# Kernel tuning notes

Hardware: AMD Instinct MI355X
Metric: run time of the kernel (lower is better)

Reference implementation:

```python
import jax, jax.numpy as jnp
import numpy as np

BN_EPS = 1e-3          # nn.BatchNorm1d(..., eps=0.001)
NUM_PILLARS = 600000   # M = total occupied pillars across the batch
N_POINTS = 3_000_000
C_IN, C_OUT = 10, 64


def setup_inputs() -> dict:
    key = jax.random.key(0)
    k1, k2, k3 = jax.random.split(key, 3)
    pts_feature = jax.random.normal(k1, (N_POINTS, C_IN), dtype=jnp.float32)
    point_pillar_indices = jax.random.randint(k2, (N_POINTS,), 0, NUM_PILLARS, dtype=jnp.int32)
    # Linear(C_IN, C_OUT, bias=False), kaiming_normal init
    W = jax.random.normal(k3, (C_IN, C_OUT), dtype=jnp.float32) * np.sqrt(2.0 / C_IN)
    # BatchNorm1d in eval mode (running stats)
    gamma = jnp.ones((C_OUT,), jnp.float32)
    beta = jnp.zeros((C_OUT,), jnp.float32)
    run_mean = jnp.zeros((C_OUT,), jnp.float32)
    run_var = jnp.ones((C_OUT,), jnp.float32)
    return {"pts_feature": pts_feature, "point_pillar_indices": point_pillar_indices,
            "W": W, "gamma": gamma, "beta": beta, "run_mean": run_mean, "run_var": run_var}


def reference(pts_feature, point_pillar_indices, W, gamma, beta, run_mean, run_var):
    # shared MLP: Linear(no bias) -> BatchNorm1d(eval) -> ReLU, fused per-point
    h = pts_feature @ W                                        # (N, C_OUT)
    h = gamma * (h - run_mean) * jax.lax.rsqrt(run_var + BN_EPS) + beta
    h = jax.nn.relu(h)
    # scatter_max over irregular pillar ids -> (M, C_OUT)
    pooled = jax.ops.segment_max(h, point_pillar_indices, num_segments=NUM_PILLARS)
    # torch scatter_max leaves empty pillars at 0; jax gives -inf -> replace
    return jnp.where(jnp.isfinite(pooled), pooled, 0.0)
```

## Files before the change

kernel.cpp:

```cpp
#include <hip/hip_runtime.h>
#include <hip/hip_bf16.h>

#define C_IN 10
#define C_OUT 64
#define BN_EPS 1e-3f

#define BPF   256
#define CB    256
#define NBMAX 4704
#define TS    2048
#define MAXT  2048

typedef __attribute__((ext_vector_type(8))) short bf16x8;
typedef __attribute__((ext_vector_type(4))) float f32x4;


__global__ __launch_bounds__(1024) void k1_hist(const int* __restrict__ idx, int n, int chunk,
                                                unsigned* __restrict__ ghist, int NB, int shift) {
    __shared__ unsigned h[NBMAX];
    const int b = blockIdx.x, t = threadIdx.x;
    for (int i = t; i < NB; i += 1024) h[i] = 0u;
    __syncthreads();
    const int lo = b * chunk;
    const int hi = min(n, lo + chunk);
    for (int i = lo + t; i < hi; i += 1024)
        atomicAdd(&h[((unsigned)idx[i]) >> shift], 1u);
    __syncthreads();
    for (int k = t; k < NB; k += 1024) ghist[(size_t)k * CB + b] = h[k];
}

__global__ __launch_bounds__(256) void k2a_reduce(const unsigned* __restrict__ g, int G,
                                                  unsigned* __restrict__ tsum) {
    __shared__ unsigned s[256];
    const int t = threadIdx.x;
    const int base = blockIdx.x * TS + t * 8;
    unsigned acc = 0;
#pragma unroll
    for (int j = 0; j < 8; ++j) { int gi = base + j; if (gi < G) acc += g[gi]; }
    s[t] = acc; __syncthreads();
    for (int off = 128; off > 0; off >>= 1) { if (t < off) s[t] += s[t + off]; __syncthreads(); }
    if (t == 0) tsum[blockIdx.x] = s[0];
}

__global__ __launch_bounds__(256) void k2b_scan(unsigned* __restrict__ tsum, int nt) {
    __shared__ unsigned partial[256], basev[256];
    const int t = threadIdx.x;
    const int per = (nt + 255) / 256;
    const int lo = t * per, hi = min(nt, lo + per);
    unsigned s = 0;
    for (int i = lo; i < hi; ++i) s += tsum[i];
    partial[t] = s; __syncthreads();
    if (t == 0) { unsigned a = 0; for (int k = 0; k < 256; ++k) { basev[k] = a; a += partial[k]; } }
    __syncthreads();
    unsigned a = basev[t];
    for (int i = lo; i < hi; ++i) { unsigned v = tsum[i]; tsum[i] = a; a += v; }
}

__global__ __launch_bounds__(256) void k2c_apply(unsigned* __restrict__ g, int G,
                                                 const unsigned* __restrict__ tsum,
                                                 unsigned* __restrict__ bstart, int NB, int n) {
    __shared__ unsigned s[256];
    const int t = threadIdx.x;
    const int base = blockIdx.x * TS + t * 8;
    unsigned v[8]; unsigned acc = 0;
#pragma unroll
    for (int j = 0; j < 8; ++j) { int gi = base + j; v[j] = (gi < G) ? g[gi] : 0u; acc += v[j]; }
    s[t] = acc; __syncthreads();
    for (int off = 1; off < 256; off <<= 1) {
        unsigned x = (t >= off) ? s[t - off] : 0u; __syncthreads();
        s[t] += x; __syncthreads();
    }
    unsigned excl = ((t == 0) ? 0u : s[t - 1]) + tsum[blockIdx.x];
#pragma unroll
    for (int j = 0; j < 8; ++j) {
        int gi = base + j;
        if (gi < G) {
            g[gi] = excl;
            if ((gi & (CB - 1)) == 0) bstart[gi / CB] = excl;
            excl += v[j];
        }
    }
    if (blockIdx.x == 0 && t == 0) bstart[NB] = (unsigned)n;
}

__global__ __launch_bounds__(1024) void k3_scatter(const int* __restrict__ idx, int n, int chunk,
                                                   const unsigned* __restrict__ scanned,
                                                   unsigned* __restrict__ rec, int NB,
                                                   int shift, unsigned lpmask) {
    __shared__ unsigned cnt[NBMAX];
    __shared__ unsigned basel[NBMAX];
    const int b = blockIdx.x, t = threadIdx.x;
    for (int k = t; k < NB; k += 1024) { basel[k] = scanned[(size_t)k * CB + b]; cnt[k] = 0u; }
    __syncthreads();
    const int lo = b * chunk, hi = min(n, lo + chunk);
    for (int i = lo + t; i < hi; i += 1024) {
        unsigned pid = (unsigned)idx[i];
        unsigned k = pid >> shift;
        unsigned r = atomicAdd(&cnt[k], 1u);
        rec[basel[k] + r] = ((pid & lpmask) << 22) | (unsigned)i;
    }
}

static __device__ __forceinline__ unsigned pk2(float2 v) {
    __hip_bfloat162 h = __float22bfloat162_rn(v);
    return *reinterpret_cast<unsigned*>(&h);
}

__global__ __launch_bounds__(1024) void pool_sfm_kernel(
    const float* __restrict__ pts,
    const unsigned* __restrict__ rec,
    const unsigned* __restrict__ bstart,
    const float* __restrict__ W,
    const float* __restrict__ gamma, const float* __restrict__ beta,
    const float* __restrict__ mean, const float* __restrict__ var,
    float* __restrict__ out, int M)
{
    __shared__ unsigned smax[BPF * C_OUT];
    __shared__ unsigned short ord[MAXT + 16];
    __shared__ unsigned lps32[(MAXT + 16) / 4];
    __shared__ unsigned cnt[BPF];
    __shared__ unsigned cur[BPF];
    __shared__ unsigned wsum[4];
    unsigned char* lpsb = (unsigned char*)lps32;

    const int b = blockIdx.x, t = threadIdx.x;
    const int lane = t & 63, w = t >> 6;
    const int g = lane >> 4, c0 = lane & 15;

    {
        uint4* s4 = (uint4*)smax;
        const uint4 z = make_uint4(0u, 0u, 0u, 0u);
        for (int i = t; i < BPF * C_OUT / 4; i += 1024) s4[i] = z;
    }
    if (t < BPF) cnt[t] = 0u;

    bf16x8 bfrag[4];
#pragma unroll
    for (int tc = 0; tc < 4; ++tc) {
        const int ch = 16 * tc + c0;
        const float sc = gamma[ch] * rsqrtf(var[ch] + BN_EPS);
        const float sh = fmaf(-mean[ch], sc, beta[ch]);
        union { bf16x8 v; unsigned short u[8]; } B;
#pragma unroll
        for (int j = 0; j < 8; ++j) {
            const int k = g * 8 + j;
            float val = 0.f;
            if (k < 10) val = W[k * C_OUT + ch] * sc;
            else if (k == 10) val = sh;
            __hip_bfloat16 hb = __float2bfloat16(val);
            B.u[j] = *reinterpret_cast<unsigned short*>(&hb);
        }
        bfrag[tc] = B.v;
    }

    const unsigned base = bstart[b];
    const int T  = (int)(bstart[b + 1] - base);
    const int Tc = T < MAXT ? T : MAXT;
    __syncthreads();

    int l0i = -1, l1i = -1;
    if (t < Tc)        { l0i = (int)(rec[base + t] >> 22);        atomicAdd(&cnt[l0i], 1u); }
    if (t + 1024 < Tc) { l1i = (int)(rec[base + t + 1024] >> 22); atomicAdd(&cnt[l1i], 1u); }
    __syncthreads();
    unsigned myv = 0, mys = 0;
    if (t < BPF) {
        myv = cnt[t];
        mys = myv;
#pragma unroll
        for (int off = 1; off < 64; off <<= 1) {
            unsigned y = (unsigned)__shfl_up((int)mys, off);
            if (lane >= off) mys += y;
        }
        if (lane == 63) wsum[t >> 6] = mys;
    }
    __syncthreads();
    if (t < BPF) {
        unsigned add = 0;
        const int mw = t >> 6;
        if (mw > 0) add += wsum[0];
        if (mw > 1) add += wsum[1];
        if (mw > 2) add += wsum[2];
        cur[t] = mys - myv + add;
    }
    __syncthreads();
    if (l0i >= 0) { unsigned p = atomicAdd(&cur[l0i], 1u); ord[p] = (unsigned short)t;          lpsb[p] = (unsigned char)l0i; }
    if (l1i >= 0) { unsigned p = atomicAdd(&cur[l1i], 1u); ord[p] = (unsigned short)(t + 1024); lpsb[p] = (unsigned char)l1i; }
    __syncthreads();
    const int nt16 = (Tc + 15) >> 4;
    {
        const int padn = nt16 * 16 - Tc;
        if (Tc > 0 && t < padn) { ord[Tc + t] = ord[Tc - 1]; lpsb[Tc + t] = lpsb[Tc - 1]; }
    }
    __syncthreads();

    int tile = w;
    unsigned rcB = 0u;
    float2 x0p, x1p, x2p, x3p, x4p;
    x0p = x1p = x2p = x3p = x4p = make_float2(0.f, 0.f);
    if (tile < nt16) {
        const int o = (int)ord[(tile << 4) + c0];
        const unsigned rcA = rec[base + o];
        const float2* fp = (const float2*)(pts + (size_t)(rcA & 0x3FFFFFu) * C_IN);
        if (g == 0)      { x0p = fp[0]; x1p = fp[1]; x2p = fp[2]; x3p = fp[3]; }
        else if (g == 1) { x4p = fp[4]; }
    }
    if (tile + 16 < nt16) {
        const int o = (int)ord[((tile + 16) << 4) + c0];
        rcB = rec[base + o];
    }

    for (; tile < nt16; tile += 16) {
        const int tb = tile << 4;
        const float2 x0 = x0p, x1 = x1p, x2 = x2p, x3 = x3p, x4 = x4p;

        unsigned rcC = 0u;
        if (tile + 32 < nt16) {
            const int o = (int)ord[((tile + 32) << 4) + c0];
            rcC = rec[base + o];
        }
        if (tile + 16 < nt16) {
            const float2* fp = (const float2*)(pts + (size_t)(rcB & 0x3FFFFFu) * C_IN);
            if (g == 0)      { x0p = fp[0]; x1p = fp[1]; x2p = fp[2]; x3p = fp[3]; }
            else if (g == 1) { x4p = fp[4]; }
        }
        rcB = rcC;

        uint4 Aq;
        if (g == 0)      Aq = make_uint4(pk2(x0), pk2(x1), pk2(x2), pk2(x3));
        else if (g == 1) Aq = make_uint4(pk2(x4), 0x00003F80u, 0u, 0u);
        else             Aq = make_uint4(0u, 0u, 0u, 0u);
        union { uint4 q; bf16x8 v; } A; A.q = Aq;

        const unsigned L = *(const unsigned*)(lpsb + tb + (g << 2));

        const f32x4 z4 = {0.f, 0.f, 0.f, 0.f};
        f32x4 a0 = __builtin_amdgcn_mfma_f32_16x16x32_bf16(A.v, bfrag[0], z4, 0, 0, 0);
        f32x4 a1 = __builtin_amdgcn_mfma_f32_16x16x32_bf16(A.v, bfrag[1], z4, 0, 0, 0);
        f32x4 a2 = __builtin_amdgcn_mfma_f32_16x16x32_bf16(A.v, bfrag[2], z4, 0, 0, 0);
        f32x4 a3 = __builtin_amdgcn_mfma_f32_16x16x32_bf16(A.v, bfrag[3], z4, 0, 0, 0);

        const int lp0 = (int)(L & 255u), lp1 = (int)((L >> 8) & 255u),
                  lp2 = (int)((L >> 16) & 255u), lp3 = (int)((L >> 24) & 255u);
        float m0 = a0[0], m1 = a1[0], m2 = a2[0], m3 = a3[0];
        int cp = lp0;
#define FLUSHM() { \
        unsigned* rowp = &smax[((unsigned)cp) << 6]; \
        const unsigned rb = (unsigned)(c0 + cp); \
        atomicMax(&rowp[(rb      ) & 63u], __float_as_uint(fmaxf(m0, 0.f))); \
        atomicMax(&rowp[(rb + 16u) & 63u], __float_as_uint(fmaxf(m1, 0.f))); \
        atomicMax(&rowp[(rb + 32u) & 63u], __float_as_uint(fmaxf(m2, 0.f))); \
        atomicMax(&rowp[(rb + 48u) & 63u], __float_as_uint(fmaxf(m3, 0.f))); }
        if (lp1 == cp) { m0 = fmaxf(m0, a0[1]); m1 = fmaxf(m1, a1[1]); m2 = fmaxf(m2, a2[1]); m3 = fmaxf(m3, a3[1]); }
        else { FLUSHM(); m0 = a0[1]; m1 = a1[1]; m2 = a2[1]; m3 = a3[1]; cp = lp1; }
        if (lp2 == cp) { m0 = fmaxf(m0, a0[2]); m1 = fmaxf(m1, a1[2]); m2 = fmaxf(m2, a2[2]); m3 = fmaxf(m3, a3[2]); }
        else { FLUSHM(); m0 = a0[2]; m1 = a1[2]; m2 = a2[2]; m3 = a3[2]; cp = lp2; }
        if (lp3 == cp) { m0 = fmaxf(m0, a0[3]); m1 = fmaxf(m1, a1[3]); m2 = fmaxf(m2, a2[3]); m3 = fmaxf(m3, a3[3]); }
        else { FLUSHM(); m0 = a0[3]; m1 = a1[3]; m2 = a2[3]; m3 = a3[3]; cp = lp3; }
        FLUSHM();
#undef FLUSHM
    }
    __syncthreads();

    for (int row = w; row < BPF; row += 16) {
        const int gp = b * BPF + row;
        if (gp < M)
            out[(size_t)gp * C_OUT + lane] = __uint_as_float(smax[row * 64 + ((lane + row) & 63)]);
    }

    if (T > MAXT) {
        __syncthreads();
        for (int r = MAXT + w; r < T; r += 16) {
            const unsigned rc = rec[base + r];
            const float* fp = pts + (size_t)(rc & 0x3FFFFFu) * C_IN;
            float h = 0.f;
#pragma unroll
            for (int j = 0; j < C_IN; ++j) h = fmaf(fp[j], W[j * C_OUT + lane], h);
            const float sc = gamma[lane] * rsqrtf(var[lane] + BN_EPS);
            h = fmaxf(fmaf(h, sc, fmaf(-mean[lane], sc, beta[lane])), 0.f);
            const int gp = b * BPF + (int)(rc >> 22);
            atomicMax((unsigned*)&out[(size_t)gp * C_OUT + lane], __float_as_uint(h));
        }
    }
}

__global__ __launch_bounds__(256) void zero_out_kernel(float4* __restrict__ out4, int n4) {
    int i = blockIdx.x * blockDim.x + threadIdx.x;
    int stride = gridDim.x * blockDim.x;
    float4 z = make_float4(0.f, 0.f, 0.f, 0.f);
    for (int j = i; j < n4; j += stride) out4[j] = z;
}

__global__ __launch_bounds__(256) void pillar_scatter_kernel(
    const float* __restrict__ pts, const int* __restrict__ idx,
    const float* __restrict__ W, const float* __restrict__ gamma,
    const float* __restrict__ beta, const float* __restrict__ mean,
    const float* __restrict__ var, unsigned int* __restrict__ out, int npoints)
{
    const int lane = threadIdx.x & 63;
    float wv[C_IN];
#pragma unroll
    for (int j = 0; j < C_IN; ++j) wv[j] = W[j * C_OUT + lane];
    const float scale = gamma[lane] * rsqrtf(var[lane] + BN_EPS);
    const float shift = fmaf(-mean[lane], scale, beta[lane]);
    const int wave_id = (blockIdx.x * blockDim.x + threadIdx.x) >> 6;
    const int nwaves  = (gridDim.x * blockDim.x) >> 6;
    for (int p = wave_id; p < npoints; p += nwaves) {
        const float* f = pts + (size_t)p * C_IN;
        float h = 0.f;
#pragma unroll
        for (int j = 0; j < C_IN; ++j) h = fmaf(f[j], wv[j], h);
        h = fmaxf(fmaf(h, scale, shift), 0.f);
        atomicMax(&out[(size_t)idx[p] * C_OUT + lane], __float_as_uint(h));
    }
}


extern "C" void kernel_launch(void* const* d_in, const int* in_sizes, int n_in,
                              void* d_out, int out_size, void* d_ws, size_t ws_size,
                              hipStream_t stream) {
    const float* pts   = (const float*)d_in[0];
    const int*   idx   = (const int*)  d_in[1];
    const float* W     = (const float*)d_in[2];
    const float* gamma = (const float*)d_in[3];
    const float* beta  = (const float*)d_in[4];
    const float* mean  = (const float*)d_in[5];
    const float* var   = (const float*)d_in[6];

    const int npoints = in_sizes[0] / C_IN;
    const int M       = out_size / C_OUT;
    const int NB      = (M + BPF - 1) / BPF;
    const int G       = NB * CB;
    const int nt      = (G + TS - 1) / TS;
    const int chunk   = (npoints + CB - 1) / CB;

    const size_t head_u32 = (size_t)G + (size_t)nt + (size_t)NB + 1;
    const size_t head_b   = ((head_u32 * 4) + 63) & ~(size_t)63;
    const size_t need     = head_b + (size_t)npoints * 4;

    if (NB <= NBMAX && npoints < (1 << 22) && nt <= 65535 && ws_size >= need) {
        unsigned* ghist  = (unsigned*)d_ws;
        unsigned* tsum   = ghist + G;
        unsigned* bstart = tsum + nt;
        unsigned* rec    = (unsigned*)((char*)d_ws + head_b);

        k1_hist        <<<CB, 1024, 0, stream>>>(idx, npoints, chunk, ghist, NB, 8);
        k2a_reduce     <<<nt, 256,  0, stream>>>(ghist, G, tsum);
        k2b_scan       <<<1,  256,  0, stream>>>(tsum, nt);
        k2c_apply      <<<nt, 256,  0, stream>>>(ghist, G, tsum, bstart, NB, npoints);
        k3_scatter     <<<CB, 1024, 0, stream>>>(idx, npoints, chunk, ghist, rec, NB, 8, 255u);
        pool_sfm_kernel<<<NB, 1024, 0, stream>>>(pts, rec, bstart, W, gamma, beta,
                                                 mean, var, (float*)d_out, M);
        return;
    }

    zero_out_kernel<<<2048, 256, 0, stream>>>((float4*)d_out, out_size / 4);
    pillar_scatter_kernel<<<2048, 256, 0, stream>>>(
        pts, idx, W, gamma, beta, mean, var, (unsigned int*)d_out, npoints);
}
```

Measured before the change: 202.5 us.

## Deepen gather prefetch to three tiles and use nontemporal stores

The pooling kernel's main loop now keeps point-feature gathers for three tiles in flight, using a rotating register triple-buffer. The record index is also fetched one further tile ahead, where before there was a single prefetched tile. Separately, the histogram, record scatter and final output writes switch to nontemporal stores to cut cache pollution. The deeper pipeline raises register pressure and may lower occupancy at 1024 threads. Nontemporal stores could hurt if the rec and ghist data are read back soon after from L2.

Result: slower. 340.3 us (+68.1%).

```diff
diff --git a/kernel.cpp b/kernel.cpp
--- a/kernel.cpp
+++ b/kernel.cpp
@@ -26,7 +26,8 @@
     for (int i = lo + t; i < hi; i += 1024)
         atomicAdd(&h[((unsigned)idx[i]) >> shift], 1u);
     __syncthreads();
-    for (int k = t; k < NB; k += 1024) ghist[(size_t)k * CB + b] = h[k];
+    for (int k = t; k < NB; k += 1024)
+        __builtin_nontemporal_store(h[k], &ghist[(size_t)k * CB + b]);
 }
 
 __global__ __launch_bounds__(256) void k2a_reduce(const unsigned* __restrict__ g, int G,
@@ -97,7 +98,7 @@
         unsigned pid = (unsigned)idx[i];
         unsigned k = pid >> shift;
         unsigned r = atomicAdd(&cnt[k], 1u);
-        rec[basel[k] + r] = ((pid & lpmask) << 22) | (unsigned)i;
+        __builtin_nontemporal_store(((pid & lpmask) << 22) | (unsigned)i, &rec[basel[k] + r]);
     }
 }
 
@@ -193,56 +194,56 @@
     }
     __syncthreads();
 
+    float2 A0, A1, A2, A3, A4, B0, B1, B2, B3, B4, E0, E1, E2, E3, E4;
+    const float2 fz = make_float2(0.f, 0.f);
+    A0 = A1 = A2 = A3 = A4 = B0 = B1 = B2 = B3 = B4 = E0 = E1 = E2 = E3 = E4 = fz;
+
+#define RECOF(TL) (((TL) < nt16) ? rec[base + (int)ord[(((TL)) << 4) + c0]] : 0u)
+#define GATHERX(P0, P1, P2, P3, P4, RC) { \
+        const float2* fp = (const float2*)(pts + (size_t)((RC) & 0x3FFFFFu) * C_IN); \
+        if (g == 0)      { P0 = fp[0]; P1 = fp[1]; P2 = fp[2]; P3 = fp[3]; } \
+        else if (g == 1) { P4 = fp[4]; } }
+
     int tile = w;
-    unsigned rcB = 0u;
-    float2 x0p, x1p, x2p, x3p, x4p;
-    x0p = x1p = x2p = x3p = x4p = make_float2(0.f, 0.f);
-    if (tile < nt16) {
-        const int o = (int)ord[(tile << 4) + c0];
-        const unsigned rcA = rec[base + o];
-        const float2* fp = (const float2*)(pts + (size_t)(rcA & 0x3FFFFFu) * C_IN);
-        if (g == 0)      { x0p = fp[0]; x1p = fp[1]; x2p = fp[2]; x3p = fp[3]; }
-        else if (g == 1) { x4p = fp[4]; }
-    }
-    if (tile + 16 < nt16) {
-        const int o = (int)ord[((tile + 16) << 4) + c0];
-        rcB = rec[base + o];
-    }
-
-    for (; tile < nt16; tile += 16) {
-        const int tb = tile << 4;
-        const float2 x0 = x0p, x1 = x1p, x2 = x2p, x3 = x3p, x4 = x4p;
-
-        unsigned rcC = 0u;
-        if (tile + 32 < nt16) {
-            const int o = (int)ord[((tile + 32) << 4) + c0];
-            rcC = rec[base + o];
-        }
-        if (tile + 16 < nt16) {
-            const float2* fp = (const float2*)(pts + (size_t)(rcB & 0x3FFFFFu) * C_IN);
-            if (g == 0)      { x0p = fp[0]; x1p = fp[1]; x2p = fp[2]; x3p = fp[3]; }
-            else if (g == 1) { x4p = fp[4]; }
-        }
-        rcB = rcC;
-
-        uint4 Aq;
-        if (g == 0)      Aq = make_uint4(pk2(x0), pk2(x1), pk2(x2), pk2(x3));
-        else if (g == 1) Aq = make_uint4(pk2(x4), 0x00003F80u, 0u, 0u);
-        else             Aq = make_uint4(0u, 0u, 0u, 0u);
-        union { uint4 q; bf16x8 v; } A; A.q = Aq;
-
-        const unsigned L = *(const unsigned*)(lpsb + tb + (g << 2));
-
-        const f32x4 z4 = {0.f, 0.f, 0.f, 0.f};
-        f32x4 a0 = __builtin_amdgcn_mfma_f32_16x16x32_bf16(A.v, bfrag[0], z4, 0, 0, 0);
-        f32x4 a1 = __builtin_amdgcn_mfma_f32_16x16x32_bf16(A.v, bfrag[1], z4, 0, 0, 0);
-        f32x4 a2 = __builtin_amdgcn_mfma_f32_16x16x32_bf16(A.v, bfrag[2], z4, 0, 0, 0);
-        f32x4 a3 = __builtin_amdgcn_mfma_f32_16x16x32_bf16(A.v, bfrag[3], z4, 0, 0, 0);
-
-        const int lp0 = (int)(L & 255u), lp1 = (int)((L >> 8) & 255u),
-                  lp2 = (int)((L >> 16) & 255u), lp3 = (int)((L >> 24) & 255u);
-        float m0 = a0[0], m1 = a1[0], m2 = a2[0], m3 = a3[0];
-        int cp = lp0;
+    {
+        const unsigned r0 = RECOF(tile);
+        const unsigned r1 = RECOF(tile + 16);
+        const unsigned r2 = RECOF(tile + 32);
+        if (tile      < nt16) GATHERX(A0, A1, A2, A3, A4, r0);
+        if (tile + 16 < nt16) GATHERX(B0, B1, B2, B3, B4, r1);
+        if (tile + 32 < nt16) GATHERX(E0, E1, E2, E3, E4, r2);
+    }
+    unsigned nrc = RECOF(tile + 48);
+
+#define COMPUTE_AND_REFILL(P0, P1, P2, P3, P4) { \
+        const int tb = tile << 4; \
+        uint4 Aq; \
+        if (g == 0)      Aq = make_uint4(pk2(P0), pk2(P1), pk2(P2), pk2(P3)); \
+        else if (g == 1) Aq = make_uint4(pk2(P4), 0x00003F80u, 0u, 0u); \
+        else             Aq = make_uint4(0u, 0u, 0u, 0u); \
+        union { uint4 q; bf16x8 v; } Au; Au.q = Aq; \
+        const unsigned L = *(const unsigned*)(lpsb + tb + (g << 2)); \
+         \
+        if (tile + 48 < nt16) GATHERX(P0, P1, P2, P3, P4, nrc); \
+        nrc = RECOF(tile + 64); \
+        const f32x4 z4 = {0.f, 0.f, 0.f, 0.f}; \
+        f32x4 a0 = __builtin_amdgcn_mfma_f32_16x16x32_bf16(Au.v, bfrag[0], z4, 0, 0, 0); \
+        f32x4 a1 = __builtin_amdgcn_mfma_f32_16x16x32_bf16(Au.v, bfrag[1], z4, 0, 0, 0); \
+        f32x4 a2 = __builtin_amdgcn_mfma_f32_16x16x32_bf16(Au.v, bfrag[2], z4, 0, 0, 0); \
+        f32x4 a3 = __builtin_amdgcn_mfma_f32_16x16x32_bf16(Au.v, bfrag[3], z4, 0, 0, 0); \
+        const int lp0 = (int)(L & 255u), lp1 = (int)((L >> 8) & 255u), \
+                  lp2 = (int)((L >> 16) & 255u), lp3 = (int)((L >> 24) & 255u); \
+        float m0 = a0[0], m1 = a1[0], m2 = a2[0], m3 = a3[0]; \
+        int cp = lp0; \
+        if (lp1 == cp) { m0 = fmaxf(m0, a0[1]); m1 = fmaxf(m1, a1[1]); m2 = fmaxf(m2, a2[1]); m3 = fmaxf(m3, a3[1]); } \
+        else { FLUSHM(); m0 = a0[1]; m1 = a1[1]; m2 = a2[1]; m3 = a3[1]; cp = lp1; } \
+        if (lp2 == cp) { m0 = fmaxf(m0, a0[2]); m1 = fmaxf(m1, a1[2]); m2 = fmaxf(m2, a2[2]); m3 = fmaxf(m3, a3[2]); } \
+        else { FLUSHM(); m0 = a0[2]; m1 = a1[2]; m2 = a2[2]; m3 = a3[2]; cp = lp2; } \
+        if (lp3 == cp) { m0 = fmaxf(m0, a0[3]); m1 = fmaxf(m1, a1[3]); m2 = fmaxf(m2, a2[3]); m3 = fmaxf(m3, a3[3]); } \
+        else { FLUSHM(); m0 = a0[3]; m1 = a1[3]; m2 = a2[3]; m3 = a3[3]; cp = lp3; } \
+        FLUSHM(); \
+        tile += 16; }
+
 #define FLUSHM() { \
         unsigned* rowp = &smax[((unsigned)cp) << 6]; \
         const unsigned rb = (unsigned)(c0 + cp); \
@@ -250,21 +251,27 @@
         atomicMax(&rowp[(rb + 16u) & 63u], __float_as_uint(fmaxf(m1, 0.f))); \
         atomicMax(&rowp[(rb + 32u) & 63u], __float_as_uint(fmaxf(m2, 0.f))); \
         atomicMax(&rowp[(rb + 48u) & 63u], __float_as_uint(fmaxf(m3, 0.f))); }
-        if (lp1 == cp) { m0 = fmaxf(m0, a0[1]); m1 = fmaxf(m1, a1[1]); m2 = fmaxf(m2, a2[1]); m3 = fmaxf(m3, a3[1]); }
-        else { FLUSHM(); m0 = a0[1]; m1 = a1[1]; m2 = a2[1]; m3 = a3[1]; cp = lp1; }
-        if (lp2 == cp) { m0 = fmaxf(m0, a0[2]); m1 = fmaxf(m1, a1[2]); m2 = fmaxf(m2, a2[2]); m3 = fmaxf(m3, a3[2]); }
-        else { FLUSHM(); m0 = a0[2]; m1 = a1[2]; m2 = a2[2]; m3 = a3[2]; cp = lp2; }
-        if (lp3 == cp) { m0 = fmaxf(m0, a0[3]); m1 = fmaxf(m1, a1[3]); m2 = fmaxf(m2, a2[3]); m3 = fmaxf(m3, a3[3]); }
-        else { FLUSHM(); m0 = a0[3]; m1 = a1[3]; m2 = a2[3]; m3 = a3[3]; cp = lp3; }
-        FLUSHM();
+
+    for (;;) {
+        if (tile >= nt16) break;
+        COMPUTE_AND_REFILL(A0, A1, A2, A3, A4);
+        if (tile >= nt16) break;
+        COMPUTE_AND_REFILL(B0, B1, B2, B3, B4);
+        if (tile >= nt16) break;
+        COMPUTE_AND_REFILL(E0, E1, E2, E3, E4);
+    }
+#undef COMPUTE_AND_REFILL
 #undef FLUSHM
-    }
+#undef GATHERX
+#undef RECOF
     __syncthreads();
 
     for (int row = w; row < BPF; row += 16) {
         const int gp = b * BPF + row;
-        if (gp < M)
-            out[(size_t)gp * C_OUT + lane] = __uint_as_float(smax[row * 64 + ((lane + row) & 63)]);
+        if (gp < M) {
+            const float v = __uint_as_float(smax[row * 64 + ((lane + row) & 63)]);
+            __builtin_nontemporal_store(v, &out[(size_t)gp * C_OUT + lane]);
+        }
     }
 
     if (T > MAXT) {
```

## Pre-gather bf16-packed point features into bucketed records during scatter

Applied to the files above, without the earlier changes.

The scatter kernel now reads each point's features sequentially, packs them to bf16 and writes them together with the local pillar id into 24-byte records in bucket order. The pooling kernel then reads these contiguous records instead of gathering fp32 point rows at random through an index. This targets random-gather inefficiency in the pool stage. In exchange it enlarges the workspace and scatter write traffic and drops the software prefetch pipeline in the pool loop.

Measured after the change: 227.7 us. 1.12x slower.

```diff
diff --git a/kernel.cpp b/kernel.cpp
--- a/kernel.cpp
+++ b/kernel.cpp
@@ -13,6 +13,7 @@
 
 typedef __attribute__((ext_vector_type(8))) short bf16x8;
 typedef __attribute__((ext_vector_type(4))) float f32x4;
+typedef unsigned long long u64;
 
 
 __global__ __launch_bounds__(1024) void k1_hist(const int* __restrict__ idx, int n, int chunk,
@@ -83,10 +84,16 @@
     if (blockIdx.x == 0 && t == 0) bstart[NB] = (unsigned)n;
 }
 
-__global__ __launch_bounds__(1024) void k3_scatter(const int* __restrict__ idx, int n, int chunk,
-                                                   const unsigned* __restrict__ scanned,
-                                                   unsigned* __restrict__ rec, int NB,
-                                                   int shift, unsigned lpmask) {
+static __device__ __forceinline__ unsigned pk2(float2 v) {
+    __hip_bfloat162 h = __float22bfloat162_rn(v);
+    return *reinterpret_cast<unsigned*>(&h);
+}
+
+__global__ __launch_bounds__(1024) void k3b_scatter_feats(
+    const int* __restrict__ idx, const float* __restrict__ pts, int n, int chunk,
+    const unsigned* __restrict__ scanned, u64* __restrict__ rec2, int NB,
+    int shift, unsigned lpmask)
+{
     __shared__ unsigned cnt[NBMAX];
     __shared__ unsigned basel[NBMAX];
     const int b = blockIdx.x, t = threadIdx.x;
@@ -94,21 +101,20 @@
     __syncthreads();
     const int lo = b * chunk, hi = min(n, lo + chunk);
     for (int i = lo + t; i < hi; i += 1024) {
-        unsigned pid = (unsigned)idx[i];
-        unsigned k = pid >> shift;
-        unsigned r = atomicAdd(&cnt[k], 1u);
-        rec[basel[k] + r] = ((pid & lpmask) << 22) | (unsigned)i;
-    }
-}
-
-static __device__ __forceinline__ unsigned pk2(float2 v) {
-    __hip_bfloat162 h = __float22bfloat162_rn(v);
-    return *reinterpret_cast<unsigned*>(&h);
-}
-
-__global__ __launch_bounds__(1024) void pool_sfm_kernel(
-    const float* __restrict__ pts,
-    const unsigned* __restrict__ rec,
+        const unsigned pid = (unsigned)idx[i];
+        const float2* f2 = (const float2*)(pts + (size_t)i * C_IN);
+        const float2 a0 = f2[0], a1 = f2[1], a2 = f2[2], a3 = f2[3], a4 = f2[4];
+        const unsigned k = pid >> shift;
+        const unsigned r = atomicAdd(&cnt[k], 1u);
+        u64* o = rec2 + (size_t)(basel[k] + r) * 3;
+        o[0] = (u64)pk2(a0) | ((u64)pk2(a1) << 32);
+        o[1] = (u64)pk2(a2) | ((u64)pk2(a3) << 32);
+        o[2] = (u64)pk2(a4) | ((u64)(pid & lpmask) << 32);
+    }
+}
+
+__global__ __launch_bounds__(1024) void pool_rec2_kernel(
+    const u64* __restrict__ rec2,
     const unsigned* __restrict__ bstart,
     const float* __restrict__ W,
     const float* __restrict__ gamma, const float* __restrict__ beta,
@@ -158,9 +164,10 @@
     const int Tc = T < MAXT ? T : MAXT;
     __syncthreads();
 
+    const unsigned* rec32 = (const unsigned*)rec2;
     int l0i = -1, l1i = -1;
-    if (t < Tc)        { l0i = (int)(rec[base + t] >> 22);        atomicAdd(&cnt[l0i], 1u); }
-    if (t + 1024 < Tc) { l1i = (int)(rec[base + t + 1024] >> 22); atomicAdd(&cnt[l1i], 1u); }
+    if (t < Tc)        { l0i = (int)(rec32[(size_t)(base + t) * 6 + 5] & 255u);        atomicAdd(&cnt[l0i], 1u); }
+    if (t + 1024 < Tc) { l1i = (int)(rec32[(size_t)(base + t + 1024) * 6 + 5] & 255u); atomicAdd(&cnt[l1i], 1u); }
     __syncthreads();
     unsigned myv = 0, mys = 0;
     if (t < BPF) {
@@ -193,41 +200,18 @@
     }
     __syncthreads();
 
-    int tile = w;
-    unsigned rcB = 0u;
-    float2 x0p, x1p, x2p, x3p, x4p;
-    x0p = x1p = x2p = x3p = x4p = make_float2(0.f, 0.f);
-    if (tile < nt16) {
-        const int o = (int)ord[(tile << 4) + c0];
-        const unsigned rcA = rec[base + o];
-        const float2* fp = (const float2*)(pts + (size_t)(rcA & 0x3FFFFFu) * C_IN);
-        if (g == 0)      { x0p = fp[0]; x1p = fp[1]; x2p = fp[2]; x3p = fp[3]; }
-        else if (g == 1) { x4p = fp[4]; }
-    }
-    if (tile + 16 < nt16) {
-        const int o = (int)ord[((tile + 16) << 4) + c0];
-        rcB = rec[base + o];
-    }
-
-    for (; tile < nt16; tile += 16) {
+    for (int tile = w; tile < nt16; tile += 16) {
         const int tb = tile << 4;
-        const float2 x0 = x0p, x1 = x1p, x2 = x2p, x3 = x3p, x4 = x4p;
-
-        unsigned rcC = 0u;
-        if (tile + 32 < nt16) {
-            const int o = (int)ord[((tile + 32) << 4) + c0];
-            rcC = rec[base + o];
-        }
-        if (tile + 16 < nt16) {
-            const float2* fp = (const float2*)(pts + (size_t)(rcB & 0x3FFFFFu) * C_IN);
-            if (g == 0)      { x0p = fp[0]; x1p = fp[1]; x2p = fp[2]; x3p = fp[3]; }
-            else if (g == 1) { x4p = fp[4]; }
-        }
-        rcB = rcC;
+        const int o = (int)ord[tb + c0];
+        const u64* r = rec2 + (size_t)(base + o) * 3;
+        u64 q0 = 0, q1 = 0, q2 = 0;
+        if (g == 0)      { q0 = r[0]; q1 = r[1]; }
+        else if (g == 1) { q2 = r[2]; }
 
         uint4 Aq;
-        if (g == 0)      Aq = make_uint4(pk2(x0), pk2(x1), pk2(x2), pk2(x3));
-        else if (g == 1) Aq = make_uint4(pk2(x4), 0x00003F80u, 0u, 0u);
+        if (g == 0)      Aq = make_uint4((unsigned)q0, (unsigned)(q0 >> 32),
+                                         (unsigned)q1, (unsigned)(q1 >> 32));
+        else if (g == 1) Aq = make_uint4((unsigned)q2, 0x00003F80u, 0u, 0u);
         else             Aq = make_uint4(0u, 0u, 0u, 0u);
         union { uint4 q; bf16x8 v; } A; A.q = Aq;
 
@@ -270,14 +254,21 @@
     if (T > MAXT) {
         __syncthreads();
         for (int r = MAXT + w; r < T; r += 16) {
-            const unsigned rc = rec[base + r];
-            const float* fp = pts + (size_t)(rc & 0x3FFFFFu) * C_IN;
+            const u64* rp = rec2 + (size_t)(base + r) * 3;
+            const u64 q0 = rp[0], q1 = rp[1], q2 = rp[2];
+            unsigned fb[5] = { (unsigned)q0, (unsigned)(q0 >> 32),
+                               (unsigned)q1, (unsigned)(q1 >> 32), (unsigned)q2 };
             float h = 0.f;
 #pragma unroll
-            for (int j = 0; j < C_IN; ++j) h = fmaf(fp[j], W[j * C_OUT + lane], h);
+            for (int j = 0; j < 5; ++j) {
+                const float flo = __uint_as_float((fb[j] & 0xFFFFu) << 16);
+                const float fhi = __uint_as_float(fb[j] & 0xFFFF0000u);
+                h = fmaf(flo, W[(2 * j) * C_OUT + lane], h);
+                h = fmaf(fhi, W[(2 * j + 1) * C_OUT + lane], h);
+            }
             const float sc = gamma[lane] * rsqrtf(var[lane] + BN_EPS);
             h = fmaxf(fmaf(h, sc, fmaf(-mean[lane], sc, beta[lane])), 0.f);
-            const int gp = b * BPF + (int)(rc >> 22);
+            const int gp = b * BPF + (int)((unsigned)(q2 >> 32) & 255u);
             atomicMax((unsigned*)&out[(size_t)gp * C_OUT + lane], __float_as_uint(h));
         }
     }
@@ -335,21 +326,22 @@
 
     const size_t head_u32 = (size_t)G + (size_t)nt + (size_t)NB + 1;
     const size_t head_b   = ((head_u32 * 4) + 63) & ~(size_t)63;
-    const size_t need     = head_b + (size_t)npoints * 4;
+    const size_t need     = head_b + (size_t)npoints * 24;
 
     if (NB <= NBMAX && npoints < (1 << 22) && nt <= 65535 && ws_size >= need) {
         unsigned* ghist  = (unsigned*)d_ws;
         unsigned* tsum   = ghist + G;
         unsigned* bstart = tsum + nt;
-        unsigned* rec    = (unsigned*)((char*)d_ws + head_b);
-
-        k1_hist        <<<CB, 1024, 0, stream>>>(idx, npoints, chunk, ghist, NB, 8);
-        k2a_reduce     <<<nt, 256,  0, stream>>>(ghist, G, tsum);
-        k2b_scan       <<<1,  256,  0, stream>>>(tsum, nt);
-        k2c_apply      <<<nt, 256,  0, stream>>>(ghist, G, tsum, bstart, NB, npoints);
-        k3_scatter     <<<CB, 1024, 0, stream>>>(idx, npoints, chunk, ghist, rec, NB, 8, 255u);
-        pool_sfm_kernel<<<NB, 1024, 0, stream>>>(pts, rec, bstart, W, gamma, beta,
-                                                 mean, var, (float*)d_out, M);
+        u64*      rec2   = (u64*)((char*)d_ws + head_b);
+
+        k1_hist          <<<CB, 1024, 0, stream>>>(idx, npoints, chunk, ghist, NB, 8);
+        k2a_reduce       <<<nt, 256,  0, stream>>>(ghist, G, tsum);
+        k2b_scan         <<<1,  256,  0, stream>>>(tsum, nt);
+        k2c_apply        <<<nt, 256,  0, stream>>>(ghist, G, tsum, bstart, NB, npoints);
+        k3b_scatter_feats<<<CB, 1024, 0, stream>>>(idx, pts, npoints, chunk, ghist,
+                                                   rec2, NB, 8, 255u);
+        pool_rec2_kernel <<<NB, 1024, 0, stream>>>(rec2, bstart, W, gamma, beta,
+                                                   mean, var, (float*)d_out, M);
         return;
     }
 
```
